# Kernel tuning notes

Measured on AMD Instinct MI355X. Metric: run time of the kernel, lower is better.

Reference implementation:

```python
import jax, jax.numpy as jnp
import numpy as np

N_WIRES = 4
N_ENT_LAYERS = 2  # params per hybrid layer have shape (2, 4)


def apply_rx(state, theta, wire):
    """Apply RX(theta) on `wire`. state: (B,2,2,2,2) complex64; theta: scalar or (B,)."""
    half = theta * 0.5
    c = jnp.cos(half).astype(jnp.complex64)
    s = (-1j) * jnp.sin(half).astype(jnp.complex64)
    moved = jnp.moveaxis(state, 1 + wire, -1)  # (B, 2,2,2, 2)
    a0, a1 = moved[..., 0], moved[..., 1]      # (B, 2,2,2)
    c = c.reshape(c.shape + (1,) * (a0.ndim - c.ndim))
    s = s.reshape(s.shape + (1,) * (a0.ndim - s.ndim))
    new = jnp.stack([c * a0 + s * a1, s * a0 + c * a1], axis=-1)
    return jnp.moveaxis(new, -1, 1 + wire)


def apply_cnot(state, control, target):
    s = jnp.moveaxis(state, [1 + control, 1 + target], [-2, -1])  # (..., 2c, 2t)
    new = jnp.stack([s[..., 0, :], s[..., 1, ::-1]], axis=-2)      # flip target where control=1
    return jnp.moveaxis(new, [-2, -1], [1 + control, 1 + target])


def expvals_z(state):
    probs = state.real ** 2 + state.imag ** 2  # (B,2,2,2,2)
    outs = []
    for w in range(N_WIRES):
        p = jnp.moveaxis(probs, 1 + w, 1)
        outs.append(jnp.sum(p[:, 0] - p[:, 1], axis=(1, 2, 3)))
    return jnp.stack(outs, axis=-1)  # (B, 4)


def qnn_batch(angles, layer_params):
    """angles: (B,4) float; layer_params: (2,4) float. Returns (B,4) Z expvals."""
    B = angles.shape[0]
    state = jnp.zeros((B,) + (2,) * N_WIRES, dtype=jnp.complex64)
    state = state.at[(slice(None),) + (0,) * N_WIRES].set(1.0)
    # AngleEmbedding (RX rotations)
    for w in range(N_WIRES):
        state = apply_rx(state, angles[:, w], w)
    # BasicEntanglerLayers: RX per wire then CNOT ring
    for l in range(N_ENT_LAYERS):
        for w in range(N_WIRES):
            state = apply_rx(state, layer_params[l, w], w)
        for w in range(N_WIRES):
            state = apply_cnot(state, w, (w + 1) % N_WIRES)
    return expvals_z(state)


def setup_inputs() -> dict:
    key = jax.random.key(0)
    ks = jax.random.split(key, 8)
    B, D_IN = 524288, 16
    inp = {
        "x": jax.random.normal(ks[0], (B, D_IN), dtype=jnp.float32),
        "theta": jax.random.normal(ks[1], (3, 2, 4), dtype=jnp.float32) * 0.01,
        "W0": jax.random.normal(ks[2], (D_IN, 4), dtype=jnp.float32) / np.sqrt(D_IN),
        "b0": jnp.zeros((4,), dtype=jnp.float32),
        "W1": jax.random.normal(ks[3], (4, 4), dtype=jnp.float32) / 2.0,
        "b1": jnp.zeros((4,), dtype=jnp.float32),
        "W2": jax.random.normal(ks[4], (4, 4), dtype=jnp.float32) / 2.0,
        "b2": jnp.zeros((4,), dtype=jnp.float32),
    }
    return inp


def reference(x, theta, W0, b0, W1, b1, W2, b2):
    Ws = [(W0, b0), (W1, b1), (W2, b2)]
    h = x
    for i, (W, b) in enumerate(Ws):
        h = jnp.tanh(h @ W + b)        # Dense + tanh
        h = qnn_batch(h, theta[i])      # vmapped 4-qubit circuit
        # Dropout(rate=0, deterministic=True) is identity
    return h
```

## Files before the change

### kernel.cpp

```cpp
#include <hip/hip_runtime.h>
#include <math.h>


__device__ __forceinline__ float fast_tanh(float x) {
    float u = __expf(2.0f * x);
    return 1.0f - 2.0f * __builtin_amdgcn_rcpf(u + 1.0f);
}

__device__ __forceinline__ void apply_rx(float2 st[16], int w, float c, float s) {
    const int bit = 1 << w;
#pragma unroll
    for (int b = 0; b < 16; ++b) {
        if (!(b & bit)) {
            float2 a0 = st[b];
            float2 a1 = st[b | bit];
            st[b].x       = fmaf(c, a0.x,  s * a1.y);
            st[b].y       = fmaf(c, a0.y, -s * a1.x);
            st[b | bit].x = fmaf(c, a1.x,  s * a0.y);
            st[b | bit].y = fmaf(c, a1.y, -s * a0.x);
        }
    }
}

__device__ __forceinline__ void apply_cnot(float2 st[16], int c, int t) {
    const int cb = 1 << c, tb = 1 << t;
#pragma unroll
    for (int b = 0; b < 16; ++b) {
        if ((b & cb) && !(b & tb)) {
            float2 tmp = st[b];
            st[b] = st[b | tb];
            st[b | tb] = tmp;
        }
    }
}

__device__ __forceinline__ void qnn(float h[4], const float* __restrict__ scL) {
    float2 st[16];
#pragma unroll
    for (int b = 0; b < 16; ++b) st[b] = make_float2(0.0f, 0.0f);
    st[0] = make_float2(1.0f, 0.0f);

#pragma unroll
    for (int w = 0; w < 4; ++w) {
        float t = 0.5f * h[w];
        apply_rx(st, w, __cosf(t), __sinf(t));
    }

#pragma unroll
    for (int l = 0; l < 2; ++l) {
#pragma unroll
        for (int w = 0; w < 4; ++w)
            apply_rx(st, w, scL[(l * 4 + w) * 2 + 0], scL[(l * 4 + w) * 2 + 1]);
#pragma unroll
        for (int w = 0; w < 4; ++w)
            apply_cnot(st, w, (w + 1) & 3);
    }

    float pr[16];
#pragma unroll
    for (int b = 0; b < 16; ++b)
        pr[b] = fmaf(st[b].x, st[b].x, st[b].y * st[b].y);

    float total = 0.0f;
#pragma unroll
    for (int b = 0; b < 16; ++b) total += pr[b];
#pragma unroll
    for (int w = 0; w < 4; ++w) {
        float s1 = 0.0f;
#pragma unroll
        for (int b = 0; b < 16; ++b)
            if ((b >> w) & 1) s1 += pr[b];
        h[w] = fmaf(-2.0f, s1, total);
    }
}

__device__ __forceinline__ void dense4(float h[4], const float* __restrict__ W,
                                       const float* __restrict__ b) {
    float g[4];
#pragma unroll
    for (int j = 0; j < 4; ++j) {
        float acc = b[j];
#pragma unroll
        for (int k = 0; k < 4; ++k) acc = fmaf(h[k], W[k * 4 + j], acc);
        g[j] = fast_tanh(acc);
    }
#pragma unroll
    for (int j = 0; j < 4; ++j) h[j] = g[j];
}

__global__ void setup_sc(const float* __restrict__ theta, float* __restrict__ sc) {
    int tid = threadIdx.x;
    if (tid < 24) {
        float t = 0.5f * theta[tid];
        sc[2 * tid + 0] = cosf(t);
        sc[2 * tid + 1] = sinf(t);
    }
}

__global__ __launch_bounds__(256)
void hqnn_kernel(const float4* __restrict__ x4,
                 const float* __restrict__ sc,
                 const float* __restrict__ W0, const float* __restrict__ b0,
                 const float* __restrict__ W1, const float* __restrict__ b1,
                 const float* __restrict__ W2, const float* __restrict__ b2,
                 float4* __restrict__ out, int B) {
    int i = blockIdx.x * blockDim.x + threadIdx.x;
    if (i >= B) return;

    float xr[16];
    float4 v0 = x4[i * 4 + 0];
    float4 v1 = x4[i * 4 + 1];
    float4 v2 = x4[i * 4 + 2];
    float4 v3 = x4[i * 4 + 3];
    xr[0] = v0.x; xr[1] = v0.y; xr[2]  = v0.z; xr[3]  = v0.w;
    xr[4] = v1.x; xr[5] = v1.y; xr[6]  = v1.z; xr[7]  = v1.w;
    xr[8] = v2.x; xr[9] = v2.y; xr[10] = v2.z; xr[11] = v2.w;
    xr[12] = v3.x; xr[13] = v3.y; xr[14] = v3.z; xr[15] = v3.w;

    float h[4];
#pragma unroll
    for (int j = 0; j < 4; ++j) {
        float acc = b0[j];
#pragma unroll
        for (int k = 0; k < 16; ++k) acc = fmaf(xr[k], W0[k * 4 + j], acc);
        h[j] = fast_tanh(acc);
    }
    qnn(h, sc + 0 * 16);

    dense4(h, W1, b1);
    qnn(h, sc + 1 * 16);

    dense4(h, W2, b2);
    qnn(h, sc + 2 * 16);

    out[i] = make_float4(h[0], h[1], h[2], h[3]);
}

extern "C" void kernel_launch(void* const* d_in, const int* in_sizes, int n_in,
                              void* d_out, int out_size, void* d_ws, size_t ws_size,
                              hipStream_t stream) {
    const float* x  = (const float*)d_in[0];
    const float* th = (const float*)d_in[1];
    const float* W0 = (const float*)d_in[2];
    const float* b0 = (const float*)d_in[3];
    const float* W1 = (const float*)d_in[4];
    const float* b1 = (const float*)d_in[5];
    const float* W2 = (const float*)d_in[6];
    const float* b2 = (const float*)d_in[7];
    float* out = (float*)d_out;
    float* sc  = (float*)d_ws;

    int B = in_sizes[0] / 16;

    hipLaunchKernelGGL(setup_sc, dim3(1), dim3(32), 0, stream, th, sc);

    int block = 256;
    int grid = (B + block - 1) / block;
    hipLaunchKernelGGL(hqnn_kernel, dim3(grid), dim3(block), 0, stream,
                       (const float4*)x, sc, W0, b0, W1, b1, W2, b2,
                       (float4*)out, B);
}
```

Measured before the change: 107.5 us.

## Replace per-sample statevector simulation with precomputed trigonometric polynomial coefficients

Each Z expectation of the circuit is a polynomial of degree at most one in cos and sin of each embedding angle. A setup kernel therefore evaluates the circuit at 81 grid points per layer and interpolates them into an 81x4 coefficient table. The main kernel then computes each layer's outputs as a tensor-product sum of cos/sin products against that table. This drops the 16-amplitude complex statevector evolution per sample, at the cost of 81 uniform float4 loads per layer and a serial single-block setup kernel. Launch bounds are also tightened to request higher occupancy.

```diff
diff --git a/kernel.cpp b/kernel.cpp
--- a/kernel.cpp
+++ b/kernel.cpp
@@ -7,7 +7,8 @@
     return 1.0f - 2.0f * __builtin_amdgcn_rcpf(u + 1.0f);
 }
 
-__device__ __forceinline__ void apply_rx(float2 st[16], int w, float c, float s) {
+
+__device__ __forceinline__ void s_apply_rx(float2 st[16], int w, float c, float s) {
     const int bit = 1 << w;
 #pragma unroll
     for (int b = 0; b < 16; ++b) {
@@ -22,7 +23,7 @@
     }
 }
 
-__device__ __forceinline__ void apply_cnot(float2 st[16], int c, int t) {
+__device__ __forceinline__ void s_apply_cnot(float2 st[16], int c, int t) {
     const int cb = 1 << c, tb = 1 << t;
 #pragma unroll
     for (int b = 0; b < 16; ++b) {
@@ -34,72 +35,80 @@
     }
 }
 
-__device__ __forceinline__ void qnn(float h[4], const float* __restrict__ scL) {
-    float2 st[16];
-#pragma unroll
-    for (int b = 0; b < 16; ++b) st[b] = make_float2(0.0f, 0.0f);
-    st[0] = make_float2(1.0f, 0.0f);
-
-#pragma unroll
-    for (int w = 0; w < 4; ++w) {
-        float t = 0.5f * h[w];
-        apply_rx(st, w, __cosf(t), __sinf(t));
-    }
-
-#pragma unroll
-    for (int l = 0; l < 2; ++l) {
-#pragma unroll
-        for (int w = 0; w < 4; ++w)
-            apply_rx(st, w, scL[(l * 4 + w) * 2 + 0], scL[(l * 4 + w) * 2 + 1]);
-#pragma unroll
-        for (int w = 0; w < 4; ++w)
-            apply_cnot(st, w, (w + 1) & 3);
-    }
-
-    float pr[16];
-#pragma unroll
-    for (int b = 0; b < 16; ++b)
-        pr[b] = fmaf(st[b].x, st[b].x, st[b].y * st[b].y);
-
-    float total = 0.0f;
-#pragma unroll
-    for (int b = 0; b < 16; ++b) total += pr[b];
-#pragma unroll
-    for (int w = 0; w < 4; ++w) {
-        float s1 = 0.0f;
-#pragma unroll
-        for (int b = 0; b < 16; ++b)
-            if ((b >> w) & 1) s1 += pr[b];
-        h[w] = fmaf(-2.0f, s1, total);
-    }
-}
-
-__device__ __forceinline__ void dense4(float h[4], const float* __restrict__ W,
-                                       const float* __restrict__ b) {
-    float g[4];
-#pragma unroll
-    for (int j = 0; j < 4; ++j) {
-        float acc = b[j];
-#pragma unroll
-        for (int k = 0; k < 4; ++k) acc = fmaf(h[k], W[k * 4 + j], acc);
-        g[j] = fast_tanh(acc);
-    }
-#pragma unroll
-    for (int j = 0; j < 4; ++j) h[j] = g[j];
-}
-
-__global__ void setup_sc(const float* __restrict__ theta, float* __restrict__ sc) {
-    int tid = threadIdx.x;
-    if (tid < 24) {
-        float t = 0.5f * theta[tid];
-        sc[2 * tid + 0] = cosf(t);
-        sc[2 * tid + 1] = sinf(t);
-    }
-}
-
-__global__ __launch_bounds__(256)
+__global__ void setup_D(const float* __restrict__ theta, float* __restrict__ D) {
+    __shared__ float bufA[81 * 4];
+    __shared__ float bufB[81 * 4];
+    const int t = threadIdx.x;
+
+    for (int layer = 0; layer < 3; ++layer) {
+        if (t < 81) {
+            const int g0 = t % 3, g1 = (t / 3) % 3, g2 = (t / 9) % 3, g3 = t / 27;
+            const float H[3] = {0.0f, 1.5707963267948966f, 3.14159265358979323f};
+            float h[4] = {H[g0], H[g1], H[g2], H[g3]};
+
+            float2 st[16];
+#pragma unroll
+            for (int b = 0; b < 16; ++b) st[b] = make_float2(0.0f, 0.0f);
+            st[0] = make_float2(1.0f, 0.0f);
+
+            for (int w = 0; w < 4; ++w)
+                s_apply_rx(st, w, cosf(0.5f * h[w]), sinf(0.5f * h[w]));
+            for (int l = 0; l < 2; ++l) {
+                for (int w = 0; w < 4; ++w) {
+                    float th = 0.5f * theta[layer * 8 + l * 4 + w];
+                    s_apply_rx(st, w, cosf(th), sinf(th));
+                }
+                for (int w = 0; w < 4; ++w)
+                    s_apply_cnot(st, w, (w + 1) & 3);
+            }
+            float pr[16], total = 0.0f;
+#pragma unroll
+            for (int b = 0; b < 16; ++b) {
+                pr[b] = st[b].x * st[b].x + st[b].y * st[b].y;
+                total += pr[b];
+            }
+            for (int w = 0; w < 4; ++w) {
+                float s1 = 0.0f;
+#pragma unroll
+                for (int b = 0; b < 16; ++b)
+                    if ((b >> w) & 1) s1 += pr[b];
+                bufA[t * 4 + w] = total - 2.0f * s1;
+            }
+        }
+        __syncthreads();
+
+        float* src = bufA;
+        float* dst = bufB;
+        int stride = 1;
+        for (int d = 0; d < 4; ++d) {
+            if (t < 81) {
+                int digit = (t / stride) % 3;
+                int base = t - digit * stride;
+                for (int c = 0; c < 4; ++c) {
+                    float y0 = src[(base + 0 * stride) * 4 + c];
+                    float y1 = src[(base + 1 * stride) * 4 + c];
+                    float y2 = src[(base + 2 * stride) * 4 + c];
+                    float m = 0.5f * (y0 + y2);
+                    float a = (digit == 0) ? m : (digit == 1) ? 0.5f * (y0 - y2) : (y1 - m);
+                    dst[t * 4 + c] = a;
+                }
+            }
+            __syncthreads();
+            float* tmp = src; src = dst; dst = tmp;
+            stride *= 3;
+        }
+        if (t < 81) {
+            for (int c = 0; c < 4; ++c)
+                D[(layer * 81 + t) * 4 + c] = src[t * 4 + c];
+        }
+        __syncthreads();
+    }
+}
+
+
+__global__ __launch_bounds__(256, 4)
 void hqnn_kernel(const float4* __restrict__ x4,
-                 const float* __restrict__ sc,
+                 const float4* __restrict__ D4,
                  const float* __restrict__ W0, const float* __restrict__ b0,
                  const float* __restrict__ W1, const float* __restrict__ b1,
                  const float* __restrict__ W2, const float* __restrict__ b2,
@@ -107,15 +116,12 @@
     int i = blockIdx.x * blockDim.x + threadIdx.x;
     if (i >= B) return;
 
-    float xr[16];
     float4 v0 = x4[i * 4 + 0];
     float4 v1 = x4[i * 4 + 1];
     float4 v2 = x4[i * 4 + 2];
     float4 v3 = x4[i * 4 + 3];
-    xr[0] = v0.x; xr[1] = v0.y; xr[2]  = v0.z; xr[3]  = v0.w;
-    xr[4] = v1.x; xr[5] = v1.y; xr[6]  = v1.z; xr[7]  = v1.w;
-    xr[8] = v2.x; xr[9] = v2.y; xr[10] = v2.z; xr[11] = v2.w;
-    xr[12] = v3.x; xr[13] = v3.y; xr[14] = v3.z; xr[15] = v3.w;
+    float xr[16] = {v0.x, v0.y, v0.z, v0.w, v1.x, v1.y, v1.z, v1.w,
+                    v2.x, v2.y, v2.z, v2.w, v3.x, v3.y, v3.z, v3.w};
 
     float h[4];
 #pragma unroll
@@ -125,13 +131,47 @@
         for (int k = 0; k < 16; ++k) acc = fmaf(xr[k], W0[k * 4 + j], acc);
         h[j] = fast_tanh(acc);
     }
-    qnn(h, sc + 0 * 16);
-
-    dense4(h, W1, b1);
-    qnn(h, sc + 1 * 16);
-
-    dense4(h, W2, b2);
-    qnn(h, sc + 2 * 16);
+
+#pragma unroll
+    for (int layer = 0; layer < 3; ++layer) {
+        if (layer > 0) {
+            const float* W = (layer == 1) ? W1 : W2;
+            const float* b = (layer == 1) ? b1 : b2;
+            float g[4];
+#pragma unroll
+            for (int j = 0; j < 4; ++j) {
+                float acc = b[j];
+#pragma unroll
+                for (int k = 0; k < 4; ++k) acc = fmaf(h[k], W[k * 4 + j], acc);
+                g[j] = fast_tanh(acc);
+            }
+#pragma unroll
+            for (int j = 0; j < 4; ++j) h[j] = g[j];
+        }
+
+        float c0 = __cosf(h[0]), s0 = __sinf(h[0]);
+        float c1 = __cosf(h[1]), s1 = __sinf(h[1]);
+        float c2 = __cosf(h[2]), s2 = __sinf(h[2]);
+        float c3 = __cosf(h[3]), s3 = __sinf(h[3]);
+
+        float p01[9] = {1.0f, c0, s0, c1, c1 * c0, c1 * s0, s1, s1 * c0, s1 * s0};
+        float p23[9] = {1.0f, c2, s2, c3, c3 * c2, c3 * s2, s3, s3 * c2, s3 * s2};
+
+        float E0 = 0.0f, E1 = 0.0f, E2 = 0.0f, E3 = 0.0f;
+#pragma unroll
+        for (int j = 0; j < 9; ++j) {
+#pragma unroll
+            for (int ii = 0; ii < 9; ++ii) {
+                float T = p01[ii] * p23[j];
+                float4 d = D4[layer * 81 + j * 9 + ii];
+                E0 = fmaf(d.x, T, E0);
+                E1 = fmaf(d.y, T, E1);
+                E2 = fmaf(d.z, T, E2);
+                E3 = fmaf(d.w, T, E3);
+            }
+        }
+        h[0] = E0; h[1] = E1; h[2] = E2; h[3] = E3;
+    }
 
     out[i] = make_float4(h[0], h[1], h[2], h[3]);
 }
@@ -148,15 +188,16 @@
     const float* W2 = (const float*)d_in[6];
     const float* b2 = (const float*)d_in[7];
     float* out = (float*)d_out;
-    float* sc  = (float*)d_ws;
+    float* D   = (float*)d_ws;
 
     int B = in_sizes[0] / 16;
 
-    hipLaunchKernelGGL(setup_sc, dim3(1), dim3(32), 0, stream, th, sc);
+    hipLaunchKernelGGL(setup_D, dim3(1), dim3(128), 0, stream, th, D);
 
     int block = 256;
     int grid = (B + block - 1) / block;
     hipLaunchKernelGGL(hqnn_kernel, dim3(grid), dim3(block), 0, stream,
-                       (const float4*)x, sc, W0, b0, W1, b1, W2, b2,
+                       (const float4*)x, (const float4*)D,
+                       W0, b0, W1, b1, W2, b2,
                        (float4*)out, B);
 }
```

After: 121.6 us. 1.13x slower.
